# Kernel tuning notes

Hardware: AMD Instinct MI355X
Metric: run time of the kernel (lower is better)

Reference implementation:

```python
import jax, jax.numpy as jnp
import numpy as np

HIDDEN = 1024

def setup_inputs() -> dict:
    key = jax.random.key(0)
    ks = jax.random.split(key, 7)
    s = 1.0 / np.sqrt(HIDDEN)
    X = jax.random.normal(ks[0], (4, 2048, HIDDEN), dtype=jnp.float32)
    Wq = jax.random.uniform(ks[1], (HIDDEN, HIDDEN), jnp.float32, -s, s)
    bq = jax.random.uniform(ks[2], (HIDDEN,), jnp.float32, -s, s)
    Wk = jax.random.uniform(ks[3], (HIDDEN, HIDDEN), jnp.float32, -s, s)
    bk = jax.random.uniform(ks[4], (HIDDEN,), jnp.float32, -s, s)
    Wv = jax.random.uniform(ks[5], (HIDDEN, HIDDEN), jnp.float32, -s, s)
    bv = jax.random.uniform(ks[6], (HIDDEN,), jnp.float32, -s, s)
    return {"X": X, "Wq": Wq, "bq": bq, "Wk": Wk, "bk": bk, "Wv": Wv, "bv": bv}

def reference(X, Wq, bq, Wk, bk, Wv, bv):
    # torch Linear: x @ W.T + b
    q = jnp.einsum('bsd,ed->bse', X, Wq) + bq  # [B,S,H]
    k = jnp.einsum('bsd,ed->bse', X, Wk) + bk
    v = jnp.einsum('bsd,ed->bse', X, Wv) + bv
    scores = jnp.einsum('bqd,bkd->bqk', q, k) / jnp.sqrt(jnp.float32(HIDDEN))  # [B,S,S]
    attn = jax.nn.softmax(scores, axis=-1)
    return jnp.einsum('bqk,bkd->bqd', attn, v)
```

## Files before the change

### kernel.cpp

```cpp
#include <hip/hip_runtime.h>
#include <hip/hip_bf16.h>
#include <stdint.h>

#define B_ 4
#define S_ 2048
#define H_ 1024

typedef __attribute__((ext_vector_type(4))) float f32x4;
typedef __attribute__((ext_vector_type(8))) short bf16x8;

#define AS1C(p) ((const __attribute__((address_space(1))) void*)(p))
#define AS3(p)  ((__attribute__((address_space(3))) void*)(p))

__global__ __launch_bounds__(256)
void prep_k(const float* __restrict__ X,
            const float* __restrict__ Wq, const float* __restrict__ Wk,
            const float* __restrict__ Wv,
            const float* __restrict__ bq, const float* __restrict__ bk,
            const float* __restrict__ bv,
            __hip_bfloat16* __restrict__ Xb, __hip_bfloat16* __restrict__ Wall,
            float* __restrict__ ball, float* __restrict__ rsum)
{
    const int NX = B_ * S_ * H_ / 4;
    const int NW = H_ * H_ / 4;
    int i = blockIdx.x * blockDim.x + threadIdx.x;
    if (i < NX + 3 * NW) {
        const float* src; uint64_t* dst; int li;
        if (i < NX) { src = X; dst = (uint64_t*)Xb; li = i; }
        else {
            int j = i - NX;
            int wsel = j / NW; li = j - wsel * NW;
            src = (wsel == 0) ? Wq : (wsel == 1) ? Wk : Wv;
            dst = (uint64_t*)Wall + (size_t)wsel * NW;
        }
        float4 v = ((const float4*)src)[li];
        union { __hip_bfloat16 h[4]; uint64_t u; } o;
        o.h[0] = __float2bfloat16(v.x);
        o.h[1] = __float2bfloat16(v.y);
        o.h[2] = __float2bfloat16(v.z);
        o.h[3] = __float2bfloat16(v.w);
        dst[li] = o.u;
    } else {
        int j = i - (NX + 3 * NW);
        if (j < 3 * H_ / 4) {
            int bsel = j >> 8;
            int off  = j & 255;
            const float* src = (bsel == 0) ? bq : (bsel == 1) ? bk : bv;
            ((float4*)ball)[j] = ((const float4*)src)[off];
        } else if (j < 3 * H_ / 4 + B_ * S_ / 4) {
            int j2 = j - 3 * H_ / 4;
            ((float4*)rsum)[j2] = make_float4(0.f, 0.f, 0.f, 0.f);
        }
    }
}

template<int BN, int MINW, bool OUT_BF16, bool HAS_BIAS, bool V_SPLIT, bool EXP_SUM, bool ROWDIV>
__global__ __launch_bounds__(256, MINW)
void gemm_bt(const __hip_bfloat16* __restrict__ A, int lda, long long aBatch,
             const __hip_bfloat16* __restrict__ B, int ldb, long long bBatch,
             const float* __restrict__ bias,
             void* __restrict__ Cout, int ldc, long long cBatch,
             __hip_bfloat16* __restrict__ vtrans, float* __restrict__ rsum,
             int M, int N, int K, float scale)
{
    constexpr int FJ = BN / 32;
    constexpr int SN = BN / 32;
    __shared__ __hip_bfloat16 lA[128 * 64];
    __shared__ __hip_bfloat16 lB[BN * 64];

    const int t  = threadIdx.x;
    const int bz = blockIdx.z;
    A += (long long)bz * aBatch;
    B += (long long)bz * bBatch;
    const int bm = blockIdx.y * 128;
    const int bn = blockIdx.x * BN;

    const int wave = t >> 6;
    const int lane = t & 63;
    const int wm = (wave & 1) * 64;
    const int wn = (wave >> 1) * (BN / 2);
    const int lm = lane & 15;
    const int kq = lane >> 4;
    const int cro = lm & 7;

    f32x4 acc[4][FJ] = {};

    const int srow = t >> 3;
    const int swz  = ((t & 7) ^ ((t >> 3) & 7)) * 8;
    const __hip_bfloat16* gA = A + (long long)(bm + srow) * lda + swz;
    const __hip_bfloat16* gB = B + (long long)(bn + srow) * ldb + swz;
    __hip_bfloat16* sA = lA + t * 8;
    __hip_bfloat16* sB = lB + t * 8;

    for (int k0 = 0; k0 < K; k0 += 64) {
        __syncthreads();
#pragma unroll
        for (int s = 0; s < 4; ++s)
            __builtin_amdgcn_global_load_lds(AS1C(gA + (long long)s * 32 * lda + k0),
                                             AS3(sA + s * 2048), 16, 0, 0);
#pragma unroll
        for (int s = 0; s < SN; ++s)
            __builtin_amdgcn_global_load_lds(AS1C(gB + (long long)s * 32 * ldb + k0),
                                             AS3(sB + s * 2048), 16, 0, 0);
        __syncthreads();

#pragma unroll
        for (int ks = 0; ks < 2; ++ks) {
            bf16x8 af[4], bfr[FJ];
            const int ch = ((ks * 4 + kq) ^ cro) * 8;
#pragma unroll
            for (int i = 0; i < 4; ++i)
                af[i] = *(const bf16x8*)(lA + (wm + i * 16 + lm) * 64 + ch);
#pragma unroll
            for (int j = 0; j < FJ; ++j)
                bfr[j] = *(const bf16x8*)(lB + (wn + j * 16 + lm) * 64 + ch);
#pragma unroll
            for (int i = 0; i < 4; ++i)
#pragma unroll
                for (int j = 0; j < FJ; ++j)
                    acc[i][j] = __builtin_amdgcn_mfma_f32_16x16x32_bf16(af[i], bfr[j], acc[i][j], 0, 0, 0);
        }
    }

    const bool vmode = V_SPLIT && (bn >= 2 * H_);
    const int r0q = kq * 4;

    if (EXP_SUM) {
#pragma unroll
        for (int i = 0; i < 4; ++i) {
            const int rowb = bm + wm + i * 16 + r0q;
            float ps[4] = {0.f, 0.f, 0.f, 0.f};
#pragma unroll
            for (int j = 0; j < FJ; ++j) {
                const int col = bn + wn + j * 16 + lm;
#pragma unroll
                for (int r = 0; r < 4; ++r) {
                    float e = __expf(acc[i][j][r] * scale);
                    ps[r] += e;
                    ((__hip_bfloat16*)Cout)[(long long)bz * cBatch +
                        (long long)(rowb + r) * ldc + col] = __float2bfloat16(e);
                }
            }
#pragma unroll
            for (int r = 0; r < 4; ++r) {
#pragma unroll
                for (int m = 1; m < 16; m <<= 1)
                    ps[r] += __shfl_xor(ps[r], m);
            }
            if (lm == 0) {
#pragma unroll
                for (int r = 0; r < 4; ++r)
                    atomicAdd(rsum + bz * S_ + rowb + r, ps[r]);
            }
        }
        return;
    }

#pragma unroll
    for (int i = 0; i < 4; ++i) {
        const int rowb = bm + wm + i * 16 + r0q;
        float inv[4];
        if (ROWDIV) {
            float4 rs = *(const float4*)(rsum + bz * S_ + rowb);
            inv[0] = 1.0f / rs.x; inv[1] = 1.0f / rs.y;
            inv[2] = 1.0f / rs.z; inv[3] = 1.0f / rs.w;
        }
#pragma unroll
        for (int j = 0; j < FJ; ++j) {
            const int col = bn + wn + j * 16 + lm;
            float bvv = 0.0f;
            if (HAS_BIAS) bvv = bias[col];
            if (!vmode) {
#pragma unroll
                for (int r = 0; r < 4; ++r) {
                    float val = ROWDIV ? acc[i][j][r] * inv[r]
                                       : acc[i][j][r] * scale + bvv;
                    long long idx = (long long)bz * cBatch + (long long)(rowb + r) * ldc + col;
                    if (OUT_BF16) ((__hip_bfloat16*)Cout)[idx] = __float2bfloat16(val);
                    else          ((float*)Cout)[idx] = val;
                }
            } else {
                const long long ebase = (long long)((rowb >> 11) * H_ + col - 2 * H_) * S_;
                union { ushort4 u; __hip_bfloat16 h[4]; } o;
#pragma unroll
                for (int r = 0; r < 4; ++r)
                    o.h[r] = __float2bfloat16(acc[i][j][r] + bvv);
                *(ushort4*)(vtrans + ebase + (rowb & 2047)) = o.u;
            }
        }
    }
}

extern "C" void kernel_launch(void* const* d_in, const int* in_sizes, int n_in,
                              void* d_out, int out_size, void* d_ws, size_t ws_size,
                              hipStream_t stream)
{
    const float* X  = (const float*)d_in[0];
    const float* Wq = (const float*)d_in[1];
    const float* bq = (const float*)d_in[2];
    const float* Wk = (const float*)d_in[3];
    const float* bk = (const float*)d_in[4];
    const float* Wv = (const float*)d_in[5];
    const float* bv = (const float*)d_in[6];
    float* out = (float*)d_out;

    char* w = (char*)d_ws;
    const size_t MB = 1ull << 20;
    __hip_bfloat16* Xb   = (__hip_bfloat16*)(w + 0);
    __hip_bfloat16* Wall = (__hip_bfloat16*)(w + 16 * MB);
    float*          ball = (float*)        (w + 22 * MB);
    __hip_bfloat16* sc   = (__hip_bfloat16*)(w + 0);
    __hip_bfloat16* qk   = (__hip_bfloat16*)(w + 32 * MB);
    __hip_bfloat16* vtb  = (__hip_bfloat16*)(w + 64 * MB);
    float*          rsum = (float*)        (w + 80 * MB);

    const int prep_items = B_ * S_ * H_ / 4 + 3 * H_ * H_ / 4 + 3 * H_ / 4 + B_ * S_ / 4;
    prep_k<<<(prep_items + 255) / 256, 256, 0, stream>>>(X, Wq, Wk, Wv, bq, bk, bv,
                                                         Xb, Wall, ball, rsum);

    dim3 g1(3 * H_ / 128, (B_ * S_) / 128, 1);
    gemm_bt<128, 1, true, true, true, false, false><<<g1, 256, 0, stream>>>(
        Xb, H_, 0, Wall, H_, 0, ball, qk, 2 * H_, 0, vtb, nullptr,
        B_ * S_, 3 * H_, H_, 1.0f);

    dim3 g2(S_ / 128, S_ / 128, B_);
    gemm_bt<128, 4, true, false, false, true, false><<<g2, 256, 0, stream>>>(
        qk,      2 * H_, (long long)S_ * 2 * H_,
        qk + H_, 2 * H_, (long long)S_ * 2 * H_,
        nullptr, sc, S_, (long long)S_ * S_, nullptr, rsum, S_, S_, H_, 0.03125f);

    dim3 g3(H_ / 64, S_ / 128, B_);
    gemm_bt<64, 4, false, false, false, false, true><<<g3, 256, 0, stream>>>(
        sc,  S_, (long long)S_ * S_,
        vtb, S_, (long long)H_ * S_,
        nullptr, out, H_, (long long)S_ * H_, nullptr, rsum, S_, H_, S_, 1.0f);
}
```

Before: 249.8 us.

## Add 256x256-tile 512-thread GEMM with 4-stage LDS pipeline for projection and scores

Introduces a new gemm256 kernel that uses 256x256 output tiles computed by 8 waves, with a 4-slot direct global-to-LDS staging ring and explicit vmcnt waits and barriers. It also raises MFMA issue priority around the compute sections. The QKV projection and QK^T score GEMMs are switched to this kernel, while the PV GEMM keeps the old one. The larger tiles are meant to raise arithmetic intensity and overlap loads with MFMAs. In exchange, the grids are smaller, register pressure is higher, and the hand-written waitcnt logic is fragile.

```diff
diff --git a/kernel.cpp b/kernel.cpp
--- a/kernel.cpp
+++ b/kernel.cpp
@@ -11,6 +11,8 @@
 
 #define AS1C(p) ((const __attribute__((address_space(1))) void*)(p))
 #define AS3(p)  ((__attribute__((address_space(3))) void*)(p))
+#define BARRIER() asm volatile("s_barrier" ::: "memory")
+#define WAITVM(n) asm volatile("s_waitcnt vmcnt(" #n ")" ::: "memory")
 
 __global__ __launch_bounds__(256)
 void prep_k(const float* __restrict__ X,
@@ -54,6 +56,163 @@
     }
 }
 
+template<bool OUT_BF16, bool HAS_BIAS, bool V_SPLIT, bool EXP_SUM>
+__global__ __launch_bounds__(512, 2)
+void gemm256(const __hip_bfloat16* __restrict__ A, int lda, long long aBatch,
+             const __hip_bfloat16* __restrict__ B, int ldb, long long bBatch,
+             const float* __restrict__ bias,
+             void* __restrict__ Cout, int ldc, long long cBatch,
+             __hip_bfloat16* __restrict__ vtrans, float* __restrict__ rsum,
+             int K, float scale)
+{
+    __shared__ __hip_bfloat16 lA[4 * 256 * 32];
+    __shared__ __hip_bfloat16 lB[4 * 256 * 32];
+
+    const int t  = threadIdx.x;
+    const int bz = blockIdx.z;
+    A += (long long)bz * aBatch;
+    B += (long long)bz * bBatch;
+    const int bm = blockIdx.y * 256;
+    const int bn = blockIdx.x * 256;
+
+    const int wave = t >> 6;
+    const int lane = t & 63;
+    const int wm = (wave >> 2) * 128;
+    const int wn = (wave & 3) * 64;
+    const int lm = lane & 15;
+    const int kq = lane >> 4;
+
+    const int srow = t >> 2;
+    const int sch  = (t & 3) ^ (srow & 3);
+    const __hip_bfloat16* gA0 = A + (long long)(bm + srow) * lda + sch * 8;
+    const __hip_bfloat16* gA1 = gA0 + (long long)128 * lda;
+    const __hip_bfloat16* gB0 = B + (long long)(bn + srow) * ldb + sch * 8;
+    const __hip_bfloat16* gB1 = gB0 + (long long)128 * ldb;
+    __hip_bfloat16* sA = lA + t * 8;
+    __hip_bfloat16* sB = lB + t * 8;
+
+    const int rch = (kq ^ (lm & 3)) * 8;
+    const __hip_bfloat16* rA = lA + (wm + lm) * 32 + rch;
+    const __hip_bfloat16* rB = lB + (wn + lm) * 32 + rch;
+
+    f32x4 acc[8][4] = {};
+    bf16x8 bfr[4];
+
+    auto stageA = [&](int js) {
+        const int so = (js & 3) * 8192;
+        __builtin_amdgcn_global_load_lds(AS1C(gA0 + js * 32), AS3(sA + so), 16, 0, 0);
+        __builtin_amdgcn_global_load_lds(AS1C(gA1 + js * 32), AS3(sA + so + 4096), 16, 0, 0);
+    };
+    auto stageB = [&](int js) {
+        const int so = (js & 3) * 8192;
+        __builtin_amdgcn_global_load_lds(AS1C(gB0 + js * 32), AS3(sB + so), 16, 0, 0);
+        __builtin_amdgcn_global_load_lds(AS1C(gB1 + js * 32), AS3(sB + so + 4096), 16, 0, 0);
+    };
+
+    stageA(0); stageB(0); stageA(1); stageB(1); stageA(2); stageB(2);
+    WAITVM(8);
+    BARRIER();
+
+    const int nIter = K >> 7;
+    for (int i = 0; i < nIter; ++i) {
+        const bool lastI = (i == nIter - 1);
+        const int j0 = i * 4;
+#pragma unroll
+        for (int p = 0; p < 8; ++p) {
+            const int slot = (p >> 1) & 3;
+            const int ch = p & 1;
+            bf16x8 af[4];
+#pragma unroll
+            for (int mi = 0; mi < 4; ++mi)
+                af[mi] = *(const bf16x8*)(rA + slot * 8192 + (ch * 4 + mi) * 512);
+            if (ch == 0) {
+#pragma unroll
+                for (int nj = 0; nj < 4; ++nj)
+                    bfr[nj] = *(const bf16x8*)(rB + slot * 8192 + nj * 512);
+            }
+            if (p < 2 || !lastI) {
+                const int js = j0 + (p >> 1) + 3;
+                if (ch == 0) stageA(js); else stageB(js);
+            }
+            BARRIER();
+            __builtin_amdgcn_s_setprio(1);
+#pragma unroll
+            for (int mi = 0; mi < 4; ++mi)
+#pragma unroll
+                for (int nj = 0; nj < 4; ++nj)
+                    acc[ch * 4 + mi][nj] = __builtin_amdgcn_mfma_f32_16x16x32_bf16(
+                        af[mi], bfr[nj], acc[ch * 4 + mi][nj], 0, 0, 0);
+            __builtin_amdgcn_s_setprio(0);
+            if (ch == 1) {
+                if (!lastI)      { WAITVM(6); }
+                else if (p == 1) { WAITVM(6); }
+                else if (p == 3) { WAITVM(4); }
+                else if (p == 5) { WAITVM(0); }
+            }
+            BARRIER();
+        }
+    }
+
+    if (EXP_SUM) {
+#pragma unroll
+        for (int fi = 0; fi < 8; ++fi) {
+            const int rowb = bm + wm + fi * 16 + kq * 4;
+            float ps[4] = {0.f, 0.f, 0.f, 0.f};
+#pragma unroll
+            for (int nj = 0; nj < 4; ++nj) {
+                const int col = bn + wn + nj * 16 + lm;
+#pragma unroll
+                for (int r = 0; r < 4; ++r) {
+                    float e = __expf(acc[fi][nj][r] * scale);
+                    ps[r] += e;
+                    ((__hip_bfloat16*)Cout)[(long long)bz * cBatch +
+                        (long long)(rowb + r) * ldc + col] = __float2bfloat16(e);
+                }
+            }
+#pragma unroll
+            for (int r = 0; r < 4; ++r) {
+#pragma unroll
+                for (int m = 1; m < 16; m <<= 1)
+                    ps[r] += __shfl_xor(ps[r], m);
+            }
+            if (lm == 0) {
+#pragma unroll
+                for (int r = 0; r < 4; ++r)
+                    atomicAdd(rsum + bz * S_ + rowb + r, ps[r]);
+            }
+        }
+        return;
+    }
+
+    const bool vmode = V_SPLIT && (bn >= 2 * H_);
+#pragma unroll
+    for (int fi = 0; fi < 8; ++fi) {
+        const int rowb = bm + wm + fi * 16 + kq * 4;
+#pragma unroll
+        for (int nj = 0; nj < 4; ++nj) {
+            const int col = bn + wn + nj * 16 + lm;
+            float bvv = 0.0f;
+            if (HAS_BIAS) bvv = bias[col];
+            if (!vmode) {
+#pragma unroll
+                for (int r = 0; r < 4; ++r) {
+                    float val = acc[fi][nj][r] * scale + bvv;
+                    long long idx = (long long)bz * cBatch + (long long)(rowb + r) * ldc + col;
+                    if (OUT_BF16) ((__hip_bfloat16*)Cout)[idx] = __float2bfloat16(val);
+                    else          ((float*)Cout)[idx] = val;
+                }
+            } else {
+                const long long ebase = (long long)((rowb >> 11) * H_ + col - 2 * H_) * S_;
+                union { ushort4 u; __hip_bfloat16 h[4]; } o;
+#pragma unroll
+                for (int r = 0; r < 4; ++r)
+                    o.h[r] = __float2bfloat16(acc[fi][nj][r] + bvv);
+                *(ushort4*)(vtrans + ebase + (rowb & 2047)) = o.u;
+            }
+        }
+    }
+}
+
 template<int BN, int MINW, bool OUT_BF16, bool HAS_BIAS, bool V_SPLIT, bool EXP_SUM, bool ROWDIV>
 __global__ __launch_bounds__(256, MINW)
 void gemm_bt(const __hip_bfloat16* __restrict__ A, int lda, long long aBatch,
@@ -218,16 +377,15 @@
     prep_k<<<(prep_items + 255) / 256, 256, 0, stream>>>(X, Wq, Wk, Wv, bq, bk, bv,
                                                          Xb, Wall, ball, rsum);
 
-    dim3 g1(3 * H_ / 128, (B_ * S_) / 128, 1);
-    gemm_bt<128, 1, true, true, true, false, false><<<g1, 256, 0, stream>>>(
-        Xb, H_, 0, Wall, H_, 0, ball, qk, 2 * H_, 0, vtb, nullptr,
-        B_ * S_, 3 * H_, H_, 1.0f);
-
-    dim3 g2(S_ / 128, S_ / 128, B_);
-    gemm_bt<128, 4, true, false, false, true, false><<<g2, 256, 0, stream>>>(
+    dim3 g1(3 * H_ / 256, (B_ * S_) / 256, 1);
+    gemm256<true, true, true, false><<<g1, 512, 0, stream>>>(
+        Xb, H_, 0, Wall, H_, 0, ball, qk, 2 * H_, 0, vtb, nullptr, H_, 1.0f);
+
+    dim3 g2(S_ / 256, S_ / 256, B_);
+    gemm256<true, false, false, true><<<g2, 512, 0, stream>>>(
         qk,      2 * H_, (long long)S_ * 2 * H_,
         qk + H_, 2 * H_, (long long)S_ * 2 * H_,
-        nullptr, sc, S_, (long long)S_ * S_, nullptr, rsum, S_, S_, H_, 0.03125f);
+        nullptr, sc, S_, (long long)S_ * S_, nullptr, rsum, H_, 0.03125f);
 
     dim3 g3(H_ / 64, S_ / 128, B_);
     gemm_bt<64, 4, false, false, false, false, true><<<g3, 256, 0, stream>>>(
```

Result: slower. 267.0 us (+6.9%).

## Add double-buffered 256-row 512-thread GEMM for score and PV stages

Applied to the files above, without the earlier changes.

Adds a new GEMM kernel that uses 512-thread blocks, 256-row tiles and double-buffered LDS staging through global_load_lds, so the load of the next K-tile overlaps the MFMA work on the current one. The QK^T (exp/sum) and PV (row-divide) launches now use this kernel with larger tiles, which raises data reuse per block and hides global load latency. In exchange it doubles LDS use and keeps a much larger accumulator array per thread, which raises register pressure and may lower occupancy. The scores grid also shrinks to 256 blocks, which is close to the CU count and may leave some CUs idle.

```diff
diff --git a/kernel.cpp b/kernel.cpp
--- a/kernel.cpp
+++ b/kernel.cpp
@@ -54,6 +54,137 @@
     }
 }
 
+template<int BN, bool OUT_BF16, bool EXP_SUM, bool ROWDIV>
+__global__ __launch_bounds__(512, 2)
+void gemm2ph(const __hip_bfloat16* __restrict__ A, int lda, long long aBatch,
+             const __hip_bfloat16* __restrict__ B, int ldb, long long bBatch,
+             void* __restrict__ Cout, int ldc, long long cBatch,
+             float* __restrict__ rsum, int K, float scale)
+{
+    constexpr int FJ = BN / 64;
+    constexpr int GB = BN / 64;
+    __shared__ __hip_bfloat16 lA[2 * 256 * 64];
+    __shared__ __hip_bfloat16 lB[2 * BN * 64];
+
+    const int t  = threadIdx.x;
+    const int bz = blockIdx.z;
+    A += (long long)bz * aBatch;
+    B += (long long)bz * bBatch;
+    const int bm = blockIdx.y * 256;
+    const int bn = blockIdx.x * BN;
+
+    const int wave = t >> 6;
+    const int lane = t & 63;
+    const int wm = (wave >> 2) * 128;
+    const int wn = (wave & 3) * (BN / 4);
+    const int lm = lane & 15;
+    const int kq = lane >> 4;
+    const int cro = lm & 7;
+
+    const int srow = t >> 3;
+    const int swz  = ((t & 7) ^ (srow & 7)) * 8;
+    const __hip_bfloat16* gA = A + (long long)(bm + srow) * lda + swz;
+    const __hip_bfloat16* gB = B + (long long)(bn + srow) * ldb + swz;
+
+    f32x4 acc[8][FJ] = {};
+
+    auto stage = [&](int buf, int k0) {
+        __hip_bfloat16* dA = lA + buf * (256 * 64) + t * 8;
+        __hip_bfloat16* dB = lB + buf * (BN * 64) + t * 8;
+#pragma unroll
+        for (int g = 0; g < 4; ++g)
+            __builtin_amdgcn_global_load_lds(AS1C(gA + (long long)g * 64 * lda + k0),
+                                             AS3(dA + g * 4096), 16, 0, 0);
+#pragma unroll
+        for (int g = 0; g < GB; ++g)
+            __builtin_amdgcn_global_load_lds(AS1C(gB + (long long)g * 64 * ldb + k0),
+                                             AS3(dB + g * 4096), 16, 0, 0);
+    };
+
+    stage(0, 0);
+    __syncthreads();
+
+    const int nT = K >> 6;
+    int buf = 0;
+    for (int tt = 0; tt < nT; ++tt) {
+        if (tt + 1 < nT) stage(buf ^ 1, (tt + 1) * 64);
+        const __hip_bfloat16* cA = lA + buf * (256 * 64) + (wm + lm) * 64;
+        const __hip_bfloat16* cB = lB + buf * (BN * 64) + (wn + lm) * 64;
+#pragma unroll
+        for (int ks = 0; ks < 2; ++ks) {
+            const int ch = ((ks * 4 + kq) ^ cro) * 8;
+            bf16x8 af[8], bfr[FJ];
+#pragma unroll
+            for (int i = 0; i < 8; ++i)
+                af[i] = *(const bf16x8*)(cA + i * 16 * 64 + ch);
+#pragma unroll
+            for (int j = 0; j < FJ; ++j)
+                bfr[j] = *(const bf16x8*)(cB + j * 16 * 64 + ch);
+#pragma unroll
+            for (int i = 0; i < 8; ++i)
+#pragma unroll
+                for (int j = 0; j < FJ; ++j)
+                    acc[i][j] = __builtin_amdgcn_mfma_f32_16x16x32_bf16(
+                        af[i], bfr[j], acc[i][j], 0, 0, 0);
+        }
+        __syncthreads();
+        buf ^= 1;
+    }
+
+    if (EXP_SUM) {
+#pragma unroll
+        for (int fi = 0; fi < 8; ++fi) {
+            const int rowb = bm + wm + fi * 16 + kq * 4;
+            float ps[4] = {0.f, 0.f, 0.f, 0.f};
+#pragma unroll
+            for (int nj = 0; nj < FJ; ++nj) {
+                const int col = bn + wn + nj * 16 + lm;
+#pragma unroll
+                for (int r = 0; r < 4; ++r) {
+                    float e = __expf(acc[fi][nj][r] * scale);
+                    ps[r] += e;
+                    ((__hip_bfloat16*)Cout)[(long long)bz * cBatch +
+                        (long long)(rowb + r) * ldc + col] = __float2bfloat16(e);
+                }
+            }
+#pragma unroll
+            for (int r = 0; r < 4; ++r) {
+#pragma unroll
+                for (int m = 1; m < 16; m <<= 1)
+                    ps[r] += __shfl_xor(ps[r], m);
+            }
+            if (lm == 0) {
+#pragma unroll
+                for (int r = 0; r < 4; ++r)
+                    atomicAdd(rsum + bz * S_ + rowb + r, ps[r]);
+            }
+        }
+        return;
+    }
+
+#pragma unroll
+    for (int fi = 0; fi < 8; ++fi) {
+        const int rowb = bm + wm + fi * 16 + kq * 4;
+        float inv[4];
+        if (ROWDIV) {
+            float4 rs = *(const float4*)(rsum + bz * S_ + rowb);
+            inv[0] = 1.0f / rs.x; inv[1] = 1.0f / rs.y;
+            inv[2] = 1.0f / rs.z; inv[3] = 1.0f / rs.w;
+        }
+#pragma unroll
+        for (int nj = 0; nj < FJ; ++nj) {
+            const int col = bn + wn + nj * 16 + lm;
+#pragma unroll
+            for (int r = 0; r < 4; ++r) {
+                float val = ROWDIV ? acc[fi][nj][r] * inv[r] : acc[fi][nj][r] * scale;
+                long long idx = (long long)bz * cBatch + (long long)(rowb + r) * ldc + col;
+                if (OUT_BF16) ((__hip_bfloat16*)Cout)[idx] = __float2bfloat16(val);
+                else          ((float*)Cout)[idx] = val;
+            }
+        }
+    }
+}
+
 template<int BN, int MINW, bool OUT_BF16, bool HAS_BIAS, bool V_SPLIT, bool EXP_SUM, bool ROWDIV>
 __global__ __launch_bounds__(256, MINW)
 void gemm_bt(const __hip_bfloat16* __restrict__ A, int lda, long long aBatch,
@@ -223,15 +354,15 @@
         Xb, H_, 0, Wall, H_, 0, ball, qk, 2 * H_, 0, vtb, nullptr,
         B_ * S_, 3 * H_, H_, 1.0f);
 
-    dim3 g2(S_ / 128, S_ / 128, B_);
-    gemm_bt<128, 4, true, false, false, true, false><<<g2, 256, 0, stream>>>(
+    dim3 g2(S_ / 256, S_ / 256, B_);
+    gemm2ph<256, true, true, false><<<g2, 512, 0, stream>>>(
         qk,      2 * H_, (long long)S_ * 2 * H_,
         qk + H_, 2 * H_, (long long)S_ * 2 * H_,
-        nullptr, sc, S_, (long long)S_ * S_, nullptr, rsum, S_, S_, H_, 0.03125f);
-
-    dim3 g3(H_ / 64, S_ / 128, B_);
-    gemm_bt<64, 4, false, false, false, false, true><<<g3, 256, 0, stream>>>(
+        sc, S_, (long long)S_ * S_, rsum, H_, 0.03125f);
+
+    dim3 g3(H_ / 128, S_ / 256, B_);
+    gemm2ph<128, false, false, true><<<g3, 512, 0, stream>>>(
         sc,  S_, (long long)S_ * S_,
         vtb, S_, (long long)H_ * S_,
-        nullptr, out, H_, (long long)S_ * H_, nullptr, rsum, S_, H_, S_, 1.0f);
+        out, H_, (long long)S_ * H_, rsum, S_, 1.0f);
 }
```

Measured after the change: 253.0 us. About the same (+1.3%).

## Fuse V projection into the score GEMM launch and grid-stride the prep kernel

Applied to the files above, without the earlier changes.

The Q/K projection is split from the V projection. V tiles are computed inside a new combined kernel that also produces the exp-scores, so both independent GEMMs share one launch and fill the GPU together. When the workspace is large enough, the scores get their own buffer so they no longer alias Xb. The prep kernel becomes a grid-stride loop with a fixed 2048-block grid, and the QK projection kernel now runs at occupancy 4 instead of 1. The cost is a workspace-size-dependent branch, and the uniform 128x128 tile mapping may balance load unevenly.

```diff
diff --git a/kernel.cpp b/kernel.cpp
--- a/kernel.cpp
+++ b/kernel.cpp
@@ -23,33 +23,36 @@
 {
     const int NX = B_ * S_ * H_ / 4;
     const int NW = H_ * H_ / 4;
-    int i = blockIdx.x * blockDim.x + threadIdx.x;
-    if (i < NX + 3 * NW) {
-        const float* src; uint64_t* dst; int li;
-        if (i < NX) { src = X; dst = (uint64_t*)Xb; li = i; }
-        else {
-            int j = i - NX;
-            int wsel = j / NW; li = j - wsel * NW;
-            src = (wsel == 0) ? Wq : (wsel == 1) ? Wk : Wv;
-            dst = (uint64_t*)Wall + (size_t)wsel * NW;
-        }
-        float4 v = ((const float4*)src)[li];
-        union { __hip_bfloat16 h[4]; uint64_t u; } o;
-        o.h[0] = __float2bfloat16(v.x);
-        o.h[1] = __float2bfloat16(v.y);
-        o.h[2] = __float2bfloat16(v.z);
-        o.h[3] = __float2bfloat16(v.w);
-        dst[li] = o.u;
-    } else {
-        int j = i - (NX + 3 * NW);
-        if (j < 3 * H_ / 4) {
-            int bsel = j >> 8;
-            int off  = j & 255;
-            const float* src = (bsel == 0) ? bq : (bsel == 1) ? bk : bv;
-            ((float4*)ball)[j] = ((const float4*)src)[off];
-        } else if (j < 3 * H_ / 4 + B_ * S_ / 4) {
-            int j2 = j - 3 * H_ / 4;
-            ((float4*)rsum)[j2] = make_float4(0.f, 0.f, 0.f, 0.f);
+    const int TOT = NX + 3 * NW + 3 * H_ / 4 + B_ * S_ / 4;
+    const int stride = gridDim.x * blockDim.x;
+    for (int i = blockIdx.x * blockDim.x + threadIdx.x; i < TOT; i += stride) {
+        if (i < NX + 3 * NW) {
+            const float* src; uint64_t* dst; int li;
+            if (i < NX) { src = X; dst = (uint64_t*)Xb; li = i; }
+            else {
+                int j = i - NX;
+                int wsel = j / NW; li = j - wsel * NW;
+                src = (wsel == 0) ? Wq : (wsel == 1) ? Wk : Wv;
+                dst = (uint64_t*)Wall + (size_t)wsel * NW;
+            }
+            float4 v = ((const float4*)src)[li];
+            union { __hip_bfloat16 h[4]; uint64_t u; } o;
+            o.h[0] = __float2bfloat16(v.x);
+            o.h[1] = __float2bfloat16(v.y);
+            o.h[2] = __float2bfloat16(v.z);
+            o.h[3] = __float2bfloat16(v.w);
+            dst[li] = o.u;
+        } else {
+            int j = i - (NX + 3 * NW);
+            if (j < 3 * H_ / 4) {
+                int bsel = j >> 8;
+                int off  = j & 255;
+                const float* src = (bsel == 0) ? bq : (bsel == 1) ? bk : bv;
+                ((float4*)ball)[j] = ((const float4*)src)[off];
+            } else {
+                int j2 = j - 3 * H_ / 4;
+                ((float4*)rsum)[j2] = make_float4(0.f, 0.f, 0.f, 0.f);
+            }
         }
     }
 }
@@ -191,6 +194,135 @@
     }
 }
 
+__global__ __launch_bounds__(256, 4)
+void sv_k(const __hip_bfloat16* __restrict__ Xb,
+          const __hip_bfloat16* __restrict__ Wall,
+          const float* __restrict__ ball,
+          const __hip_bfloat16* __restrict__ qk,
+          __hip_bfloat16* __restrict__ sc,
+          __hip_bfloat16* __restrict__ vtb,
+          float* __restrict__ rsum)
+{
+    __shared__ __hip_bfloat16 lA[128 * 64];
+    __shared__ __hip_bfloat16 lB[128 * 64];
+
+    const int t  = threadIdx.x;
+    const int id = blockIdx.x;
+    const bool vrole = (id % 3) == 0;
+
+    const __hip_bfloat16 *A, *Bm;
+    int lda, ldb, bm, bn, bz = 0;
+    if (vrole) {
+        const int v = id / 3;
+        bm = (v >> 3) * 128;
+        bn = 2 * H_ + (v & 7) * 128;
+        A  = Xb;   lda = H_;
+        Bm = Wall; ldb = H_;
+    } else {
+        const int s = id - id / 3 - 1;
+        bz = s >> 8;
+        bm = ((s >> 4) & 15) * 128;
+        bn = (s & 15) * 128;
+        A  = qk      + (long long)bz * S_ * 2 * H_;
+        Bm = qk + H_ + (long long)bz * S_ * 2 * H_;
+        lda = 2 * H_; ldb = 2 * H_;
+    }
+
+    const int wave = t >> 6;
+    const int lane = t & 63;
+    const int wm = (wave & 1) * 64;
+    const int wn = (wave >> 1) * 64;
+    const int lm = lane & 15;
+    const int kq = lane >> 4;
+    const int cro = lm & 7;
+
+    f32x4 acc[4][4] = {};
+
+    const int srow = t >> 3;
+    const int swz  = ((t & 7) ^ ((t >> 3) & 7)) * 8;
+    const __hip_bfloat16* gA = A  + (long long)(bm + srow) * lda + swz;
+    const __hip_bfloat16* gB = Bm + (long long)(bn + srow) * ldb + swz;
+    __hip_bfloat16* sA = lA + t * 8;
+    __hip_bfloat16* sB = lB + t * 8;
+
+    for (int k0 = 0; k0 < H_; k0 += 64) {
+        __syncthreads();
+#pragma unroll
+        for (int s = 0; s < 4; ++s)
+            __builtin_amdgcn_global_load_lds(AS1C(gA + (long long)s * 32 * lda + k0),
+                                             AS3(sA + s * 2048), 16, 0, 0);
+#pragma unroll
+        for (int s = 0; s < 4; ++s)
+            __builtin_amdgcn_global_load_lds(AS1C(gB + (long long)s * 32 * ldb + k0),
+                                             AS3(sB + s * 2048), 16, 0, 0);
+        __syncthreads();
+
+#pragma unroll
+        for (int ks = 0; ks < 2; ++ks) {
+            bf16x8 af[4], bfr[4];
+            const int ch = ((ks * 4 + kq) ^ cro) * 8;
+#pragma unroll
+            for (int i = 0; i < 4; ++i)
+                af[i] = *(const bf16x8*)(lA + (wm + i * 16 + lm) * 64 + ch);
+#pragma unroll
+            for (int j = 0; j < 4; ++j)
+                bfr[j] = *(const bf16x8*)(lB + (wn + j * 16 + lm) * 64 + ch);
+#pragma unroll
+            for (int i = 0; i < 4; ++i)
+#pragma unroll
+                for (int j = 0; j < 4; ++j)
+                    acc[i][j] = __builtin_amdgcn_mfma_f32_16x16x32_bf16(af[i], bfr[j], acc[i][j], 0, 0, 0);
+        }
+    }
+
+    const int r0q = kq * 4;
+    if (vrole) {
+#pragma unroll
+        for (int i = 0; i < 4; ++i) {
+            const int rowb = bm + wm + i * 16 + r0q;
+#pragma unroll
+            for (int j = 0; j < 4; ++j) {
+                const int col = bn + wn + j * 16 + lm;
+                const float bvv = ball[col];
+                const long long ebase = (long long)((rowb >> 11) * H_ + col - 2 * H_) * S_;
+                union { ushort4 u; __hip_bfloat16 h[4]; } o;
+#pragma unroll
+                for (int r = 0; r < 4; ++r)
+                    o.h[r] = __float2bfloat16(acc[i][j][r] + bvv);
+                *(ushort4*)(vtb + ebase + (rowb & 2047)) = o.u;
+            }
+        }
+    } else {
+#pragma unroll
+        for (int i = 0; i < 4; ++i) {
+            const int rowb = bm + wm + i * 16 + r0q;
+            float ps[4] = {0.f, 0.f, 0.f, 0.f};
+#pragma unroll
+            for (int j = 0; j < 4; ++j) {
+                const int col = bn + wn + j * 16 + lm;
+#pragma unroll
+                for (int r = 0; r < 4; ++r) {
+                    float e = __expf(acc[i][j][r] * 0.03125f);
+                    ps[r] += e;
+                    sc[(long long)bz * S_ * S_ + (long long)(rowb + r) * S_ + col] =
+                        __float2bfloat16(e);
+                }
+            }
+#pragma unroll
+            for (int r = 0; r < 4; ++r) {
+#pragma unroll
+                for (int m = 1; m < 16; m <<= 1)
+                    ps[r] += __shfl_xor(ps[r], m);
+            }
+            if (lm == 0) {
+#pragma unroll
+                for (int r = 0; r < 4; ++r)
+                    atomicAdd(rsum + bz * S_ + rowb + r, ps[r]);
+            }
+        }
+    }
+}
+
 extern "C" void kernel_launch(void* const* d_in, const int* in_sizes, int n_in,
                               void* d_out, int out_size, void* d_ws, size_t ws_size,
                               hipStream_t stream)
@@ -206,28 +338,37 @@
 
     char* w = (char*)d_ws;
     const size_t MB = 1ull << 20;
+    const bool big = ws_size >= 113 * MB;
     __hip_bfloat16* Xb   = (__hip_bfloat16*)(w + 0);
     __hip_bfloat16* Wall = (__hip_bfloat16*)(w + 16 * MB);
     float*          ball = (float*)        (w + 22 * MB);
-    __hip_bfloat16* sc   = (__hip_bfloat16*)(w + 0);
     __hip_bfloat16* qk   = (__hip_bfloat16*)(w + 32 * MB);
     __hip_bfloat16* vtb  = (__hip_bfloat16*)(w + 64 * MB);
-    float*          rsum = (float*)        (w + 80 * MB);
-
-    const int prep_items = B_ * S_ * H_ / 4 + 3 * H_ * H_ / 4 + 3 * H_ / 4 + B_ * S_ / 4;
-    prep_k<<<(prep_items + 255) / 256, 256, 0, stream>>>(X, Wq, Wk, Wv, bq, bk, bv,
-                                                         Xb, Wall, ball, rsum);
-
-    dim3 g1(3 * H_ / 128, (B_ * S_) / 128, 1);
-    gemm_bt<128, 1, true, true, true, false, false><<<g1, 256, 0, stream>>>(
-        Xb, H_, 0, Wall, H_, 0, ball, qk, 2 * H_, 0, vtb, nullptr,
-        B_ * S_, 3 * H_, H_, 1.0f);
-
-    dim3 g2(S_ / 128, S_ / 128, B_);
-    gemm_bt<128, 4, true, false, false, true, false><<<g2, 256, 0, stream>>>(
-        qk,      2 * H_, (long long)S_ * 2 * H_,
-        qk + H_, 2 * H_, (long long)S_ * 2 * H_,
-        nullptr, sc, S_, (long long)S_ * S_, nullptr, rsum, S_, S_, H_, 0.03125f);
+    __hip_bfloat16* sc   = big ? (__hip_bfloat16*)(w + 80 * MB) : (__hip_bfloat16*)(w + 0);
+    float*          rsum = big ? (float*)(w + 112 * MB)         : (float*)(w + 80 * MB);
+
+    prep_k<<<2048, 256, 0, stream>>>(X, Wq, Wk, Wv, bq, bk, bv,
+                                     Xb, Wall, ball, rsum);
+
+    if (big) {
+        dim3 g1(2 * H_ / 128, (B_ * S_) / 128, 1);
+        gemm_bt<128, 4, true, true, true, false, false><<<g1, 256, 0, stream>>>(
+            Xb, H_, 0, Wall, H_, 0, ball, qk, 2 * H_, 0, vtb, nullptr,
+            B_ * S_, 2 * H_, H_, 1.0f);
+
+        sv_k<<<1536, 256, 0, stream>>>(Xb, Wall, ball, qk, sc, vtb, rsum);
+    } else {
+        dim3 g1(3 * H_ / 128, (B_ * S_) / 128, 1);
+        gemm_bt<128, 1, true, true, true, false, false><<<g1, 256, 0, stream>>>(
+            Xb, H_, 0, Wall, H_, 0, ball, qk, 2 * H_, 0, vtb, nullptr,
+            B_ * S_, 3 * H_, H_, 1.0f);
+
+        dim3 g2(S_ / 128, S_ / 128, B_);
+        gemm_bt<128, 4, true, false, false, true, false><<<g2, 256, 0, stream>>>(
+            qk,      2 * H_, (long long)S_ * 2 * H_,
+            qk + H_, 2 * H_, (long long)S_ * 2 * H_,
+            nullptr, sc, S_, (long long)S_ * S_, nullptr, rsum, S_, S_, H_, 0.03125f);
+    }
 
     dim3 g3(H_ / 64, S_ / 128, B_);
     gemm_bt<64, 4, false, false, false, false, true><<<g3, 256, 0, stream>>>(
```

Result: slower. 314.5 us (+25.9%).
